# Kernel tuning notes

Measured on AMD Instinct MI355X. Metric: run time of the kernel, lower is better.

The kernel has to match this reference:

```python
import jax, jax.numpy as jnp
import numpy as np

N, E = 50000, 800000
IN_DIM, E_DIM, OUT_DIM, H = 128, 32, 16, 4
NEG_SLOPE = 0.2


def setup_inputs() -> dict:
    key = jax.random.key(0)
    ks = jax.random.split(key, 9)
    return {
        "feat": jax.random.normal(ks[0], (N, IN_DIM), jnp.float32),
        "edge_attr": jax.random.normal(ks[1], (E, E_DIM), jnp.float32),
        "src": jax.random.randint(ks[2], (E,), 0, N),
        "dst": jax.random.randint(ks[3], (E,), 0, N),
        "W_fc": jax.random.normal(ks[4], (OUT_DIM * H, IN_DIM), jnp.float32) * 0.1,
        "W_edge": jax.random.normal(ks[5], (OUT_DIM * H, E_DIM), jnp.float32) * 0.1,
        "attn_h": jax.random.normal(ks[6], (1, H, OUT_DIM), jnp.float32) * 0.1,
        "attn_t": jax.random.normal(ks[7], (1, H, OUT_DIM), jnp.float32) * 0.1,
        "attn_e": jax.random.normal(ks[8], (1, H, OUT_DIM), jnp.float32) * 0.1,
        "bias": jnp.zeros((1, H, OUT_DIM), jnp.float32),
    }


def reference(feat, edge_attr, src, dst, W_fc, W_edge, attn_h, attn_t, attn_e, bias):
    n = feat.shape[0]
    # node / edge projections
    feat_ = (feat @ W_fc.T).reshape(n, H, OUT_DIM)          # [N,H,D]
    eh = (feat_ * attn_h).sum(-1)                            # [N,H]
    et = (feat_ * attn_t).sum(-1)                            # [N,H]
    feat_e = (edge_attr @ W_edge.T).reshape(-1, H, OUT_DIM)  # [E,H,D]
    ee = (feat_e * attn_e).sum(-1)                           # [E,H]
    # per-edge attention logits: u_add_e then e_add_v, then leaky relu
    e = eh[src] + ee + et[dst]                               # [E,H]
    e = jnp.where(e > 0, e, NEG_SLOPE * e)
    # edge softmax grouped by destination node
    e_max = jax.ops.segment_max(e, dst, num_segments=n)      # [N,H]
    e_max = jnp.where(jnp.isfinite(e_max), e_max, 0.0)
    a = jnp.exp(e - e_max[dst])                              # [E,H]
    a_sum = jax.ops.segment_sum(a, dst, num_segments=n)      # [N,H]
    a = a / jnp.where(a_sum[dst] > 0, a_sum[dst], 1.0)
    # u_mul_e + sum aggregation
    msg = feat_[src] * a[:, :, None]                         # [E,H,D]
    rst = jax.ops.segment_sum(msg, dst, num_segments=n)      # [N,H,D]
    rst = rst + bias
    return rst.reshape(n, H * OUT_DIM)                       # concat_out
```

## Files before the change

kernel.cpp:

```cpp
#include <hip/hip_runtime.h>

#define NN 50000
#define EE 800000
#define IND 128
#define EDD 32
#define ODD 16
#define NH 4
#define HD 64
#define NEG_SLOPE 0.2f
#define NBLK ((NN + 255) / 256)

typedef float  f32x4 __attribute__((ext_vector_type(4)));
typedef int    i32x2 __attribute__((ext_vector_type(2)));
typedef _Float16 f16x8 __attribute__((ext_vector_type(8)));

__global__ __launch_bounds__(256)
void k_init_prep(int* __restrict__ deg, const float* __restrict__ W_fc,
                 const float* __restrict__ W_edge, const float* __restrict__ attn_e,
                 float* __restrict__ Wt, float* __restrict__ w_ee) {
    int i = blockIdx.x * 256 + threadIdx.x;
    if (i < NN) deg[i] = 0;
    if (i < HD * IND) {
        int k = i >> 6, j = i & 63;
        Wt[i] = W_fc[j * IND + k];
    }
    if (i < NH * EDD) {
        int h = i >> 5, k = i & 31;
        float s = 0.f;
        for (int d = 0; d < ODD; ++d)
            s += W_edge[(h * ODD + d) * EDD + k] * attn_e[h * ODD + d];
        w_ee[i] = s;
    }
}

__global__ __launch_bounds__(256)
void k_node(const float* __restrict__ feat, const float* __restrict__ Wt,
            const float* __restrict__ attn_h, const float* __restrict__ attn_t,
            _Float16* __restrict__ feat_h, float2* __restrict__ eh2,
            float2* __restrict__ et2) {
    int n = blockIdx.x * 256 + threadIdx.x;
    int hf = blockIdx.y;
    if (n >= NN) return;
    const int jbase = hf * 32;
    f32x4 row[32];
    const f32x4* fr4 = (const f32x4*)(feat + (long)n * IND);
#pragma unroll
    for (int q = 0; q < 32; ++q) row[q] = __builtin_nontemporal_load(fr4 + q);
    asm volatile("" ::: "memory");
    float acc[32];
#pragma unroll
    for (int j = 0; j < 32; ++j) acc[j] = 0.f;
#pragma unroll
    for (int k0 = 0; k0 < 32; ++k0) {
        float f[4] = {row[k0][0], row[k0][1], row[k0][2], row[k0][3]};
#pragma unroll
        for (int kk = 0; kk < 4; ++kk) {
            const float* w = Wt + (k0 * 4 + kk) * HD + jbase;
#pragma unroll
            for (int j = 0; j < 32; ++j) acc[j] += f[kk] * w[j];
        }
    }
    f16x8* d8 = (f16x8*)(feat_h + (long)n * HD + jbase);
#pragma unroll
    for (int q = 0; q < 4; ++q) {
        f16x8 v;
#pragma unroll
        for (int j = 0; j < 8; ++j) v[j] = (_Float16)acc[q * 8 + j];
        d8[q] = v;
    }
    float sh[2], st[2];
#pragma unroll
    for (int hh = 0; hh < 2; ++hh) {
        sh[hh] = 0.f; st[hh] = 0.f;
        int hg = hf * 2 + hh;
#pragma unroll
        for (int d = 0; d < ODD; ++d) {
            float av = acc[hh * ODD + d];
            sh[hh] += av * attn_h[hg * ODD + d];
            st[hh] += av * attn_t[hg * ODD + d];
        }
    }
    eh2[n * 2 + hf] = make_float2(sh[0], sh[1]);
    et2[n * 2 + hf] = make_float2(st[0], st[1]);
}

__global__ __launch_bounds__(256)
void k_hist(const int* __restrict__ dst, int* __restrict__ deg, int* __restrict__ rank) {
    int e = blockIdx.x * 256 + threadIdx.x;
    if (e < EE) {
        int d = __builtin_nontemporal_load(dst + e);
        rank[e] = atomicAdd(&deg[d], 1);
    }
}

__global__ __launch_bounds__(256)
void k_scan1(const int* __restrict__ deg, int* __restrict__ offs, int* __restrict__ part) {
    __shared__ int s[256];
    int t = threadIdx.x, i = blockIdx.x * 256 + t;
    int v = (i < NN) ? deg[i] : 0;
    s[t] = v;
    __syncthreads();
#pragma unroll
    for (int o = 1; o < 256; o <<= 1) {
        int u = (t >= o) ? s[t - o] : 0;
        __syncthreads();
        if (t >= o) s[t] += u;
        __syncthreads();
    }
    if (i < NN) offs[i] = s[t] - v;
    if (t == 255) part[blockIdx.x] = s[255];
}

__global__ __launch_bounds__(256)
void k_scan2(int* __restrict__ part) {
    __shared__ int s[256];
    int t = threadIdx.x;
    int v = (t < NBLK) ? part[t] : 0;
    s[t] = v;
    __syncthreads();
#pragma unroll
    for (int o = 1; o < 256; o <<= 1) {
        int u = (t >= o) ? s[t - o] : 0;
        __syncthreads();
        if (t >= o) s[t] += u;
        __syncthreads();
    }
    if (t < NBLK) part[t] = s[t] - v;
}

__global__ __launch_bounds__(256)
void k_scan3(int* __restrict__ offs, const int* __restrict__ part) {
    int i = blockIdx.x * 256 + threadIdx.x;
    if (i < NN) offs[i] += part[i >> 8];
}

__global__ __launch_bounds__(256)
void k_edge(const float* __restrict__ edge_attr, const int* __restrict__ dst,
            const int* __restrict__ src, const float* __restrict__ w_ee,
            const int* __restrict__ offs, const int* __restrict__ rank,
            const float4* __restrict__ eh4, const float4* __restrict__ et4,
            float4* __restrict__ a4, int* __restrict__ asrc) {
    int t = blockIdx.x * 256 + threadIdx.x;
    int e0 = t * 2;
    if (e0 >= EE) return;
    i32x2 d2 = __builtin_nontemporal_load((const i32x2*)(dst + e0));
    i32x2 r2 = __builtin_nontemporal_load((const i32x2*)(rank + e0));
    i32x2 s2 = __builtin_nontemporal_load((const i32x2*)(src + e0));
    int o0 = offs[d2[0]], o1 = offs[d2[1]];
    const f32x4* ea = (const f32x4*)(edge_attr + (long)e0 * EDD);
    f32x4 r[16];
#pragma unroll
    for (int c = 0; c < 16; ++c) r[c] = __builtin_nontemporal_load(ea + c);
    asm volatile("" ::: "memory");
    float4 eh0 = eh4[s2[0]], eh1 = eh4[s2[1]];
    float4 et0 = et4[d2[0]], et1 = et4[d2[1]];
    float he0[4] = {eh0.x + et0.x, eh0.y + et0.y, eh0.z + et0.z, eh0.w + et0.w};
    float he1[4] = {eh1.x + et1.x, eh1.y + et1.y, eh1.z + et1.z, eh1.w + et1.w};
    const float* f0 = (const float*)&r[0];
    const float* f1 = (const float*)&r[8];
    float a0[NH], a1[NH];
#pragma unroll
    for (int h = 0; h < NH; ++h) {
        float a = 0.f, b = 0.f;
#pragma unroll
        for (int k = 0; k < EDD; ++k) {
            float w = w_ee[h * EDD + k];
            a += f0[k] * w;
            b += f1[k] * w;
        }
        a += he0[h]; b += he1[h];
        a = a > 0.f ? a : NEG_SLOPE * a;
        b = b > 0.f ? b : NEG_SLOPE * b;
        a0[h] = __expf(a);
        a1[h] = __expf(b);
    }
    int p0 = o0 + r2[0], p1 = o1 + r2[1];
    a4[p0] = make_float4(a0[0], a0[1], a0[2], a0[3]);
    a4[p1] = make_float4(a1[0], a1[1], a1[2], a1[3]);
    asrc[p0] = s2[0];
    asrc[p1] = s2[1];
}

__global__ __launch_bounds__(256)
void k_reduce(const int* __restrict__ offs, const int* __restrict__ deg,
              const float* __restrict__ a_f, const int* __restrict__ asrc,
              const _Float16* __restrict__ feat_h, const float* __restrict__ bias,
              float* __restrict__ out) {
    int wid = (blockIdx.x * 256 + threadIdx.x) >> 6;
    int lane = threadIdx.x & 63;
    if (wid >= NN) return;
    int start = __builtin_amdgcn_readfirstlane(offs[wid]);
    int dn    = __builtin_amdgcn_readfirstlane(deg[wid]);
    int h = lane >> 4;
    int q = lane & 15;
    float acc = 0.f, l = 0.f;

    for (int c0 = 0; c0 < dn; c0 += 16) {
        int rem = dn - c0; if (rem > 16) rem = 16;
        int qq = (q < rem) ? q : (rem - 1);
        int pos = start + c0 + qq;
        int   s_q = asrc[pos];
        float a_q = a_f[(long)pos * 4 + h];
        if (q >= rem) a_q = 0.f;
        float f[16];
#pragma unroll
        for (int i = 0; i < 16; ++i) {
            int si = __shfl(s_q, i);
            f[i] = (float)feat_h[(long)si * HD + lane];
        }
#pragma unroll
        for (int i = 0; i < 16; ++i) {
            float ai = __shfl(a_q, (lane & 48) + i);
            l += ai;
            acc += ai * f[i];
        }
    }
    float res = (l > 0.f) ? acc / l : 0.f;
    __builtin_nontemporal_store(res + bias[lane], &out[(long)wid * HD + lane]);
}

extern "C" void kernel_launch(void* const* d_in, const int* in_sizes, int n_in,
                              void* d_out, int out_size, void* d_ws, size_t ws_size,
                              hipStream_t stream) {
    const float* feat      = (const float*)d_in[0];
    const float* edge_attr = (const float*)d_in[1];
    const int*   src       = (const int*)d_in[2];
    const int*   dst       = (const int*)d_in[3];
    const float* W_fc      = (const float*)d_in[4];
    const float* W_edge    = (const float*)d_in[5];
    const float* attn_h    = (const float*)d_in[6];
    const float* attn_t    = (const float*)d_in[7];
    const float* attn_e    = (const float*)d_in[8];
    const float* bias      = (const float*)d_in[9];
    float* out             = (float*)d_out;

    float* ws        = (float*)d_ws;
    float4* a4       = (float4*)ws;
    float4* eh4      = a4 + EE;
    float4* et4      = eh4 + NN;
    _Float16* feat_h = (_Float16*)(et4 + NN);
    float*  Wt       = (float*)(feat_h + (long)NN * HD);
    float*  w_ee     = Wt + HD * IND;
    int*    asrc     = (int*)(w_ee + NH * EDD);
    int*    rank     = asrc + EE;
    int*    deg      = rank + EE;
    int*    offs     = deg + NN;
    int*    part     = offs + NN;

    k_init_prep<<<NBLK, 256, 0, stream>>>(deg, W_fc, W_edge, attn_e, Wt, w_ee);
    dim3 ngrid(NBLK, 2);
    k_node<<<ngrid, 256, 0, stream>>>(feat, Wt, attn_h, attn_t, feat_h,
                                      (float2*)eh4, (float2*)et4);
    k_hist<<<(EE + 255) / 256, 256, 0, stream>>>(dst, deg, rank);
    k_scan1<<<NBLK, 256, 0, stream>>>(deg, offs, part);
    k_scan2<<<1, 256, 0, stream>>>(part);
    k_scan3<<<NBLK, 256, 0, stream>>>(offs, part);
    k_edge<<<(EE / 2 + 255) / 256, 256, 0, stream>>>(edge_attr, dst, src, w_ee,
                                                     offs, rank, eh4, et4, a4, asrc);
    k_reduce<<<(NN * 64 + 255) / 256, 256, 0, stream>>>(offs, deg, (const float*)a4,
                                                        asrc, feat_h, bias, out);
}
```

Baseline: 383.4 us.

## Write coalesced per-edge records and scatter only a permutation index

k_edge now writes each edge's source index and fp16-packed attention weights as a 16-byte record in edge order, using coalesced nontemporal stores. It scatters only a 4-byte edge id into a CSR-ordered permutation array, replacing the earlier scattered float4 plus int writes. k_reduce reads the permutation and then gathers the record, which adds one level of indirection and a random 16-byte read per edge. Attention weights drop to fp16 precision, and the nontemporal load hints on dst, rank and src are removed.

```diff
diff --git a/kernel.cpp b/kernel.cpp
--- a/kernel.cpp
+++ b/kernel.cpp
@@ -12,7 +12,10 @@
 
 typedef float  f32x4 __attribute__((ext_vector_type(4)));
 typedef int    i32x2 __attribute__((ext_vector_type(2)));
+typedef int    i32x4 __attribute__((ext_vector_type(4)));
 typedef _Float16 f16x8 __attribute__((ext_vector_type(8)));
+
+union h2i { int i; _Float16 h[2]; };
 
 __global__ __launch_bounds__(256)
 void k_init_prep(int* __restrict__ deg, const float* __restrict__ W_fc,
@@ -87,10 +90,7 @@
 __global__ __launch_bounds__(256)
 void k_hist(const int* __restrict__ dst, int* __restrict__ deg, int* __restrict__ rank) {
     int e = blockIdx.x * 256 + threadIdx.x;
-    if (e < EE) {
-        int d = __builtin_nontemporal_load(dst + e);
-        rank[e] = atomicAdd(&deg[d], 1);
-    }
+    if (e < EE) rank[e] = atomicAdd(&deg[dst[e]], 1);
 }
 
 __global__ __launch_bounds__(256)
@@ -139,13 +139,13 @@
             const int* __restrict__ src, const float* __restrict__ w_ee,
             const int* __restrict__ offs, const int* __restrict__ rank,
             const float4* __restrict__ eh4, const float4* __restrict__ et4,
-            float4* __restrict__ a4, int* __restrict__ asrc) {
+            i32x4* __restrict__ rec4, int* __restrict__ perm) {
     int t = blockIdx.x * 256 + threadIdx.x;
     int e0 = t * 2;
     if (e0 >= EE) return;
-    i32x2 d2 = __builtin_nontemporal_load((const i32x2*)(dst + e0));
-    i32x2 r2 = __builtin_nontemporal_load((const i32x2*)(rank + e0));
-    i32x2 s2 = __builtin_nontemporal_load((const i32x2*)(src + e0));
+    i32x2 d2 = *(const i32x2*)(dst + e0);
+    i32x2 r2 = *(const i32x2*)(rank + e0);
+    i32x2 s2 = *(const i32x2*)(src + e0);
     int o0 = offs[d2[0]], o1 = offs[d2[1]];
     const f32x4* ea = (const f32x4*)(edge_attr + (long)e0 * EDD);
     f32x4 r[16];
@@ -174,16 +174,22 @@
         a0[h] = __expf(a);
         a1[h] = __expf(b);
     }
-    int p0 = o0 + r2[0], p1 = o1 + r2[1];
-    a4[p0] = make_float4(a0[0], a0[1], a0[2], a0[3]);
-    a4[p1] = make_float4(a1[0], a1[1], a1[2], a1[3]);
-    asrc[p0] = s2[0];
-    asrc[p1] = s2[1];
+    h2i p01, p23, q01, q23;
+    p01.h[0] = (_Float16)a0[0]; p01.h[1] = (_Float16)a0[1];
+    p23.h[0] = (_Float16)a0[2]; p23.h[1] = (_Float16)a0[3];
+    q01.h[0] = (_Float16)a1[0]; q01.h[1] = (_Float16)a1[1];
+    q23.h[0] = (_Float16)a1[2]; q23.h[1] = (_Float16)a1[3];
+    i32x4 rc0 = {s2[0], p01.i, p23.i, 0};
+    i32x4 rc1 = {s2[1], q01.i, q23.i, 0};
+    __builtin_nontemporal_store(rc0, rec4 + e0);
+    __builtin_nontemporal_store(rc1, rec4 + e0 + 1);
+    perm[o0 + r2[0]] = e0;
+    perm[o1 + r2[1]] = e0 + 1;
 }
 
 __global__ __launch_bounds__(256)
 void k_reduce(const int* __restrict__ offs, const int* __restrict__ deg,
-              const float* __restrict__ a_f, const int* __restrict__ asrc,
+              const i32x4* __restrict__ rec4, const int* __restrict__ perm,
               const _Float16* __restrict__ feat_h, const float* __restrict__ bias,
               float* __restrict__ out) {
     int wid = (blockIdx.x * 256 + threadIdx.x) >> 6;
@@ -198,9 +204,11 @@
     for (int c0 = 0; c0 < dn; c0 += 16) {
         int rem = dn - c0; if (rem > 16) rem = 16;
         int qq = (q < rem) ? q : (rem - 1);
-        int pos = start + c0 + qq;
-        int   s_q = asrc[pos];
-        float a_q = a_f[(long)pos * 4 + h];
+        int   e_q = perm[start + c0 + qq];
+        i32x4 r   = rec4[e_q];
+        int   s_q = r.x;
+        h2i u; u.i = (h & 2) ? r.z : r.y;
+        float a_q = (float)u.h[h & 1];
         if (q >= rem) a_q = 0.f;
         float f[16];
 #pragma unroll
@@ -235,14 +243,14 @@
     float* out             = (float*)d_out;
 
     float* ws        = (float*)d_ws;
-    float4* a4       = (float4*)ws;
-    float4* eh4      = a4 + EE;
+    i32x4*  rec4     = (i32x4*)ws;
+    float4* eh4      = (float4*)(rec4 + EE);
     float4* et4      = eh4 + NN;
     _Float16* feat_h = (_Float16*)(et4 + NN);
     float*  Wt       = (float*)(feat_h + (long)NN * HD);
     float*  w_ee     = Wt + HD * IND;
-    int*    asrc     = (int*)(w_ee + NH * EDD);
-    int*    rank     = asrc + EE;
+    int*    perm     = (int*)(w_ee + NH * EDD);
+    int*    rank     = perm + EE;
     int*    deg      = rank + EE;
     int*    offs     = deg + NN;
     int*    part     = offs + NN;
@@ -256,7 +264,7 @@
     k_scan2<<<1, 256, 0, stream>>>(part);
     k_scan3<<<NBLK, 256, 0, stream>>>(offs, part);
     k_edge<<<(EE / 2 + 255) / 256, 256, 0, stream>>>(edge_attr, dst, src, w_ee,
-                                                     offs, rank, eh4, et4, a4, asrc);
-    k_reduce<<<(NN * 64 + 255) / 256, 256, 0, stream>>>(offs, deg, (const float*)a4,
-                                                        asrc, feat_h, bias, out);
-}
+                                                     offs, rank, eh4, et4, rec4, perm);
+    k_reduce<<<(NN * 64 + 255) / 256, 256, 0, stream>>>(offs, deg, rec4, perm,
+                                                        feat_h, bias, out);
+}
```

New measurement: 387.4 us. Within noise of the previous version (+1.0%).

## Split edge pipeline: coalesced edge-score kernel, atomic-cursor permutation, logits in reduce

Applied to the files above, without the earlier changes.

The fused edge kernel is split in two. One kernel computes the per-edge attention projection from edge_attr and writes it in original edge order with coalesced stores. A separate permutation kernel uses atomic cursors to build (edge id, src) records in CSR order, replacing the separate rank array. The reduce kernel then gathers the edge score by edge id, adds the eh/et terms, and applies leaky-relu and exp itself. This replaces scattered 16-byte writes per edge with coalesced ones, at the cost of an extra random gather of za4 in reduce and one more kernel launch.

```diff
diff --git a/kernel.cpp b/kernel.cpp
--- a/kernel.cpp
+++ b/kernel.cpp
@@ -85,12 +85,9 @@
 }
 
 __global__ __launch_bounds__(256)
-void k_hist(const int* __restrict__ dst, int* __restrict__ deg, int* __restrict__ rank) {
+void k_hist(const int* __restrict__ dst, int* __restrict__ deg) {
     int e = blockIdx.x * 256 + threadIdx.x;
-    if (e < EE) {
-        int d = __builtin_nontemporal_load(dst + e);
-        rank[e] = atomicAdd(&deg[d], 1);
-    }
+    if (e < EE) atomicAdd(&deg[__builtin_nontemporal_load(dst + e)], 1);
 }
 
 __global__ __launch_bounds__(256)
@@ -129,36 +126,30 @@
 }
 
 __global__ __launch_bounds__(256)
-void k_scan3(int* __restrict__ offs, const int* __restrict__ part) {
+void k_scan3(int* __restrict__ offs, int* __restrict__ cursor,
+             const int* __restrict__ part) {
     int i = blockIdx.x * 256 + threadIdx.x;
-    if (i < NN) offs[i] += part[i >> 8];
-}
-
-__global__ __launch_bounds__(256)
-void k_edge(const float* __restrict__ edge_attr, const int* __restrict__ dst,
-            const int* __restrict__ src, const float* __restrict__ w_ee,
-            const int* __restrict__ offs, const int* __restrict__ rank,
-            const float4* __restrict__ eh4, const float4* __restrict__ et4,
-            float4* __restrict__ a4, int* __restrict__ asrc) {
+    if (i < NN) {
+        int v = offs[i] + part[i >> 8];
+        offs[i] = v;
+        cursor[i] = v;
+    }
+}
+
+__global__ __launch_bounds__(256)
+void k_ee(const float* __restrict__ edge_attr, const float* __restrict__ w_ee,
+          f32x4* __restrict__ za4) {
     int t = blockIdx.x * 256 + threadIdx.x;
     int e0 = t * 2;
     if (e0 >= EE) return;
-    i32x2 d2 = __builtin_nontemporal_load((const i32x2*)(dst + e0));
-    i32x2 r2 = __builtin_nontemporal_load((const i32x2*)(rank + e0));
-    i32x2 s2 = __builtin_nontemporal_load((const i32x2*)(src + e0));
-    int o0 = offs[d2[0]], o1 = offs[d2[1]];
     const f32x4* ea = (const f32x4*)(edge_attr + (long)e0 * EDD);
     f32x4 r[16];
 #pragma unroll
     for (int c = 0; c < 16; ++c) r[c] = __builtin_nontemporal_load(ea + c);
     asm volatile("" ::: "memory");
-    float4 eh0 = eh4[s2[0]], eh1 = eh4[s2[1]];
-    float4 et0 = et4[d2[0]], et1 = et4[d2[1]];
-    float he0[4] = {eh0.x + et0.x, eh0.y + et0.y, eh0.z + et0.z, eh0.w + et0.w};
-    float he1[4] = {eh1.x + et1.x, eh1.y + et1.y, eh1.z + et1.z, eh1.w + et1.w};
     const float* f0 = (const float*)&r[0];
     const float* f1 = (const float*)&r[8];
-    float a0[NH], a1[NH];
+    f32x4 z0, z1;
 #pragma unroll
     for (int h = 0; h < NH; ++h) {
         float a = 0.f, b = 0.f;
@@ -168,22 +159,28 @@
             a += f0[k] * w;
             b += f1[k] * w;
         }
-        a += he0[h]; b += he1[h];
-        a = a > 0.f ? a : NEG_SLOPE * a;
-        b = b > 0.f ? b : NEG_SLOPE * b;
-        a0[h] = __expf(a);
-        a1[h] = __expf(b);
-    }
-    int p0 = o0 + r2[0], p1 = o1 + r2[1];
-    a4[p0] = make_float4(a0[0], a0[1], a0[2], a0[3]);
-    a4[p1] = make_float4(a1[0], a1[1], a1[2], a1[3]);
-    asrc[p0] = s2[0];
-    asrc[p1] = s2[1];
+        z0[h] = a; z1[h] = b;
+    }
+    __builtin_nontemporal_store(z0, za4 + e0);
+    __builtin_nontemporal_store(z1, za4 + e0 + 1);
+}
+
+__global__ __launch_bounds__(256)
+void k_perm(const int* __restrict__ dst, const int* __restrict__ src,
+            int* __restrict__ cursor, i32x2* __restrict__ perm2) {
+    int e = blockIdx.x * 256 + threadIdx.x;
+    if (e >= EE) return;
+    int d = __builtin_nontemporal_load(dst + e);
+    int s = __builtin_nontemporal_load(src + e);
+    int pos = atomicAdd(&cursor[d], 1);
+    i32x2 rec = {e, s};
+    __builtin_nontemporal_store(rec, perm2 + pos);
 }
 
 __global__ __launch_bounds__(256)
 void k_reduce(const int* __restrict__ offs, const int* __restrict__ deg,
-              const float* __restrict__ a_f, const int* __restrict__ asrc,
+              const f32x4* __restrict__ za4, const i32x2* __restrict__ perm2,
+              const float* __restrict__ eh, const float* __restrict__ et,
               const _Float16* __restrict__ feat_h, const float* __restrict__ bias,
               float* __restrict__ out) {
     int wid = (blockIdx.x * 256 + threadIdx.x) >> 6;
@@ -193,15 +190,19 @@
     int dn    = __builtin_amdgcn_readfirstlane(deg[wid]);
     int h = lane >> 4;
     int q = lane & 15;
+    float et_h = et[(long)wid * 4 + h];
     float acc = 0.f, l = 0.f;
 
     for (int c0 = 0; c0 < dn; c0 += 16) {
         int rem = dn - c0; if (rem > 16) rem = 16;
         int qq = (q < rem) ? q : (rem - 1);
-        int pos = start + c0 + qq;
-        int   s_q = asrc[pos];
-        float a_q = a_f[(long)pos * 4 + h];
-        if (q >= rem) a_q = 0.f;
+        i32x2 p = perm2[start + c0 + qq];
+        int e_q = p.x, s_q = p.y;
+        float z   = za4[e_q][h];
+        float ehv = eh[(long)s_q * 4 + h];
+        float x = z + ehv + et_h;
+        x = x > 0.f ? x : NEG_SLOPE * x;
+        float a_q = (q < rem) ? __expf(x) : 0.f;
         float f[16];
 #pragma unroll
         for (int i = 0; i < 16; ++i) {
@@ -235,28 +236,30 @@
     float* out             = (float*)d_out;
 
     float* ws        = (float*)d_ws;
-    float4* a4       = (float4*)ws;
-    float4* eh4      = a4 + EE;
+    f32x4*  za4      = (f32x4*)ws;
+    float4* eh4      = (float4*)(za4 + EE);
     float4* et4      = eh4 + NN;
     _Float16* feat_h = (_Float16*)(et4 + NN);
     float*  Wt       = (float*)(feat_h + (long)NN * HD);
     float*  w_ee     = Wt + HD * IND;
-    int*    asrc     = (int*)(w_ee + NH * EDD);
-    int*    rank     = asrc + EE;
-    int*    deg      = rank + EE;
+    i32x2*  perm2    = (i32x2*)(w_ee + NH * EDD);
+    int*    deg      = (int*)(perm2 + EE);
     int*    offs     = deg + NN;
-    int*    part     = offs + NN;
+    int*    cursor   = offs + NN;
+    int*    part     = cursor + NN;
 
     k_init_prep<<<NBLK, 256, 0, stream>>>(deg, W_fc, W_edge, attn_e, Wt, w_ee);
     dim3 ngrid(NBLK, 2);
     k_node<<<ngrid, 256, 0, stream>>>(feat, Wt, attn_h, attn_t, feat_h,
                                       (float2*)eh4, (float2*)et4);
-    k_hist<<<(EE + 255) / 256, 256, 0, stream>>>(dst, deg, rank);
+    k_ee<<<(EE / 2 + 255) / 256, 256, 0, stream>>>(edge_attr, w_ee, za4);
+    k_hist<<<(EE + 255) / 256, 256, 0, stream>>>(dst, deg);
     k_scan1<<<NBLK, 256, 0, stream>>>(deg, offs, part);
     k_scan2<<<1, 256, 0, stream>>>(part);
-    k_scan3<<<NBLK, 256, 0, stream>>>(offs, part);
-    k_edge<<<(EE / 2 + 255) / 256, 256, 0, stream>>>(edge_attr, dst, src, w_ee,
-                                                     offs, rank, eh4, et4, a4, asrc);
-    k_reduce<<<(NN * 64 + 255) / 256, 256, 0, stream>>>(offs, deg, (const float*)a4,
-                                                        asrc, feat_h, bias, out);
-}
+    k_scan3<<<NBLK, 256, 0, stream>>>(offs, cursor, part);
+    k_perm<<<(EE + 255) / 256, 256, 0, stream>>>(dst, src, cursor, perm2);
+    k_reduce<<<(NN * 64 + 255) / 256, 256, 0, stream>>>(offs, deg, za4, perm2,
+                                                        (const float*)eh4,
+                                                        (const float*)et4,
+                                                        feat_h, bias, out);
+}
```

New measurement: 406.6 us. 6.1% more time.
